# Kernel optimization log

Measured on AMD Instinct MI355X. Metric: run time of the kernel, lower is better.

The kernel has to match this reference:

```python
import jax, jax.numpy as jnp
import numpy as np

DIM_X = 256
DIM_V = 512
DIM_IN = 2
N = 65536
EPS = 0.05          # posdef_tol
CRLB = 0.0          # contraction_rate_lb
STD = 0.5           # weight_init_std


def setup_inputs() -> dict:
    key = jax.random.key(0)
    ks = jax.random.split(key, 8)
    return {
        "t": 0,
        "x": jax.random.normal(ks[0], (N, DIM_X), jnp.float32),
        "Pstar": jax.random.normal(ks[1], (DIM_X, DIM_X), jnp.float32) * STD,
        "Chi": jax.random.normal(ks[2], (DIM_X, DIM_V), jnp.float32) * STD,
        "X": jax.random.normal(ks[3], (DIM_X + DIM_V, DIM_X + DIM_V), jnp.float32) * STD,
        "Y1": jax.random.normal(ks[4], (DIM_X, DIM_X), jnp.float32) * STD,
        "B2": jax.random.normal(ks[5], (DIM_X, DIM_IN), jnp.float32) * STD,
        "D12": jax.random.normal(ks[6], (DIM_V, DIM_IN), jnp.float32) * STD,
        "bv": jnp.zeros((DIM_V,), jnp.float32),
        "bx": jnp.zeros((DIM_X,), jnp.float32),
    }


def _model_matrices(Pstar, Chi, X, Y1):
    """Replicates CREN.update_model_param (F.linear(a,b) == a @ b.T)."""
    dx = Pstar.shape[0]
    P = 0.5 * (Pstar @ Pstar.T) + EPS * jnp.eye(dx, dtype=Pstar.dtype)
    H = X @ X.T + EPS * jnp.eye(X.shape[0], dtype=X.dtype)
    H1 = H[:dx, :dx]
    H2 = H[:dx, dx:]
    H4 = H[dx:, dx:]
    Y = -0.5 * (H1 + CRLB * P + Y1 - Y1.T)
    lam = 0.5 * jnp.diagonal(H4)                 # Lambda is diagonal
    Pinv = jnp.linalg.inv(P)
    A = Pinv @ Y                                  # F.linear(inv(P), Y.T)
    D11 = -jnp.tril(H4, -1) / lam[:, None]        # strictly lower triangular
    C1 = Chi.T / lam[:, None]                     # (dv, dx)
    B1 = Pinv @ (-H2 - Chi)                       # (dx, dv)
    return A, B1, C1, D11


def reference(t, x, Pstar, Chi, X, Y1, B2, D12, bv, bx):
    A, B1, C1, D11 = _model_matrices(Pstar, Chi, X, Y1)
    n = x.shape[0]
    u = jnp.zeros((1, DIM_IN), x.dtype)           # hard-coded zero input in forward
    # precompute the per-step linear terms that do not depend on w:
    # cx[:, i] == F.linear(x, C1[i]) + bv[i] + F.linear(u, D12[i])
    cx = x @ C1.T + bv[None, :] + u @ D12.T       # (n, dv)

    idx = jnp.arange(DIM_V)

    def step(w, xs):
        i, cxi, d_row = xs                        # cxi: (n,), d_row: (dv,)
        v = cxi + w @ d_row                       # forward substitution step
        w = w.at[:, i].set(jnp.tanh(v))
        return w, None

    w0 = jnp.zeros((n, DIM_V), x.dtype)
    w, _ = jax.lax.scan(step, w0, (idx, cx.T, D11))

    x_dot = x @ A.T + w @ B1.T + bx[None, :] + u @ B2.T
    return x_dot


if __name__ == "__main__":
    out = reference(**setup_inputs())
    print(out.shape, out.dtype)
```

## Files before the change

kernel.cpp:

```cpp
#include <hip/hip_runtime.h>
#include <cstdint>
#include <cstddef>

#define DIMX 256
#define DIMV 512
#define DIMH 768
#define EPSV 0.05f

typedef __bf16 bf16x8 __attribute__((ext_vector_type(8)));
typedef unsigned short u16x8 __attribute__((ext_vector_type(8)));
typedef unsigned int u32x4 __attribute__((ext_vector_type(4)));
typedef float f32x4 __attribute__((ext_vector_type(4)));

__device__ __forceinline__ unsigned short f2bf(float f) {
  unsigned int u = __float_as_uint(f);
  u += 0x7fffu + ((u >> 16) & 1u);
  return (unsigned short)(u >> 16);
}
__device__ __forceinline__ float bf2f(unsigned short b) {
  return __uint_as_float(((unsigned int)b) << 16);
}
__device__ __forceinline__ bf16x8 ld8(const unsigned short* p) {
  u16x8 u = *reinterpret_cast<const u16x8*>(p);
  return __builtin_bit_cast(bf16x8, u);
}
__device__ __forceinline__ f32x4 mfma16(bf16x8 a, bf16x8 b, f32x4 c) {
  return __builtin_amdgcn_mfma_f32_16x16x32_bf16(a, b, c, 0, 0, 0);
}
__device__ __forceinline__ float rdlane(float v, int lane) {
  return __uint_as_float(
      (unsigned int)__builtin_amdgcn_readlane((int)__float_as_uint(v), lane));
}

__global__ __launch_bounds__(256) void k_setup1(const float* __restrict__ X,
                                                unsigned short* __restrict__ Xhi,
                                                unsigned short* __restrict__ Xlo,
                                                const float* __restrict__ Pst,
                                                float* __restrict__ P) {
  int blk = blockIdx.x;
  if (blk < 256) {
    int bi = blk >> 4, bj = blk & 15;
    int ty = threadIdx.x >> 4, tx = threadIdx.x & 15;
    int i = bi * 16 + ty, j = bj * 16 + tx;
    const f32x4* ra = reinterpret_cast<const f32x4*>(Pst + (size_t)i * DIMX);
    const f32x4* rb = reinterpret_cast<const f32x4*>(Pst + (size_t)j * DIMX);
    float s = 0.f;
    for (int k = 0; k < 64; ++k) {
      f32x4 a = ra[k], b = rb[k];
      s = fmaf(a[0], b[0], s); s = fmaf(a[1], b[1], s);
      s = fmaf(a[2], b[2], s); s = fmaf(a[3], b[3], s);
    }
    P[(size_t)i * DIMX + j] = 0.5f * s + (i == j ? EPSV : 0.f);
  } else {
    int idx = (blk - 256) * 256 + threadIdx.x;
    if (idx < DIMH * DIMH) {
      float f = X[idx];
      unsigned short h = f2bf(f);
      Xhi[idx] = h;
      Xlo[idx] = f2bf(f - bf2f(h));
    }
  }
}

__global__ __launch_bounds__(256, 1) void k_setup2(float* __restrict__ A,
                                                   float* __restrict__ Wbuf,
                                                   const unsigned short* __restrict__ Xhi,
                                                   const unsigned short* __restrict__ Xlo,
                                                   float* __restrict__ H) {
  __shared__ float Wl[32][33];
  __shared__ float T[32][232];
  if (blockIdx.x == 0) {
    int t = threadIdx.x;
    int wv = t >> 6, l = t & 63;
#pragma unroll 1
    for (int s = 0; s < 8; ++s) {
      int K = 32 * s;
      int R32 = 256 - K - 32;
      if (wv == 0) {
        int li = l & 31;
        float d[32];
#pragma unroll
        for (int j = 0; j < 32; ++j) d[j] = A[(K + j) * 256 + K + li];
#pragma unroll
        for (int k = 0; k < 32; ++k) {
          float dkk = rdlane(d[k], k);
          float ip = rsqrtf(dkk);
          d[k] *= ip;
#pragma unroll
          for (int j = k + 1; j < 32; ++j) {
            float ljk = rdlane(d[k], j);
            d[j] = fmaf(-ljk, d[k], d[j]);
          }
        }
        float wcol[32];
#pragma unroll
        for (int i = 0; i < 32; ++i) {
          float Lii = rdlane(d[i], i);
          float ipi = 1.0f / Lii;
          float acc = (li == i) ? 1.0f : 0.0f;
#pragma unroll
          for (int k = 0; k < i; ++k) {
            float Lik = rdlane(d[k], i);
            acc = fmaf(-Lik, wcol[k], acc);
          }
          wcol[i] = acc * ipi;
        }
        if (l < 32) {
#pragma unroll
          for (int k = 0; k < 32; ++k) {
            Wl[k][l] = wcol[k];
            Wbuf[s * 1024 + k * 32 + l] = wcol[k];
          }
        }
      }
      __syncthreads();
      if (R32 > 0) {
        int nrt = R32 >> 2;
        for (int u = t; u < nrt * 8; u += 256) {
          int rt = u >> 3, jg = u & 7;
          int r = K + 32 + rt * 4;
          int j0 = jg * 4;
          f32x4 z4 = {0.f, 0.f, 0.f, 0.f};
          f32x4 acc[4] = {z4, z4, z4, z4};
#pragma unroll
          for (int k = 0; k < 32; ++k) {
            f32x4 av = *reinterpret_cast<const f32x4*>(&A[(K + k) * 256 + r]);
#pragma unroll
            for (int jj = 0; jj < 4; ++jj) {
              float w = Wl[j0 + jj][k];
              acc[jj][0] = fmaf(av[0], w, acc[jj][0]);
              acc[jj][1] = fmaf(av[1], w, acc[jj][1]);
              acc[jj][2] = fmaf(av[2], w, acc[jj][2]);
              acc[jj][3] = fmaf(av[3], w, acc[jj][3]);
            }
          }
#pragma unroll
          for (int jj = 0; jj < 4; ++jj)
            *reinterpret_cast<f32x4*>(&T[j0 + jj][rt * 4]) = acc[jj];
        }
        __syncthreads();
#pragma unroll 1
        for (int j = 0; j < 32; ++j) {
          int rl = t << 2;
          if (rl < R32)
            *reinterpret_cast<f32x4*>(&A[(K + j) * 256 + K + 32 + rl]) =
                *reinterpret_cast<const f32x4*>(&T[j][rl]);
        }
        int T4 = R32 >> 2;
        int ntile = T4 * (T4 + 1) / 2;
        for (int idx = t; idx < ntile; idx += 256) {
          int ti = (int)((sqrtf(8.0f * (float)idx + 1.0f) - 1.0f) * 0.5f);
          while ((ti + 1) * (ti + 2) / 2 <= idx) ++ti;
          while (ti * (ti + 1) / 2 > idx) --ti;
          int tj = idx - ti * (ti + 1) / 2;
          int gi = K + 32 + 4 * ti, gj = K + 32 + 4 * tj;
          f32x4 acc[4];
#pragma unroll
          for (int jj = 0; jj < 4; ++jj)
            acc[jj] = *reinterpret_cast<const f32x4*>(&A[(gj + jj) * 256 + gi]);
#pragma unroll
          for (int k = 0; k < 32; ++k) {
            f32x4 av = *reinterpret_cast<const f32x4*>(&T[k][4 * ti]);
            f32x4 bv = *reinterpret_cast<const f32x4*>(&T[k][4 * tj]);
#pragma unroll
            for (int jj = 0; jj < 4; ++jj) {
              acc[jj][0] = fmaf(-av[0], bv[jj], acc[jj][0]);
              acc[jj][1] = fmaf(-av[1], bv[jj], acc[jj][1]);
              acc[jj][2] = fmaf(-av[2], bv[jj], acc[jj][2]);
              acc[jj][3] = fmaf(-av[3], bv[jj], acc[jj][3]);
            }
          }
#pragma unroll
          for (int jj = 0; jj < 4; ++jj)
            *reinterpret_cast<f32x4*>(&A[(gj + jj) * 256 + gi]) = acc[jj];
        }
      }
      __syncthreads();
    }
  } else {
    int b2 = blockIdx.x - 1;
    int bx = b2 % 12, by = b2 / 12;
    int i0 = by * 64, j0 = bx * 64;
    int l = threadIdx.x & 63, wv = threadIdx.x >> 6;
    int lr = l & 15, lq = l >> 4;
    int koff = lq * 8;
    int arow = i0 + wv * 16 + lr;
    f32x4 z = {0.f, 0.f, 0.f, 0.f};
    f32x4 acc[4] = {z, z, z, z};
    for (int pass = 0; pass < 3; ++pass) {
      const unsigned short* Xa = (pass == 2) ? Xlo : Xhi;
      const unsigned short* Xb = (pass == 1) ? Xlo : Xhi;
      for (int kc = 0; kc < 24; ++kc) {
        bf16x8 a = ld8(&Xa[(size_t)arow * DIMH + kc * 32 + koff]);
#pragma unroll
        for (int ct = 0; ct < 4; ++ct) {
          bf16x8 b = ld8(&Xb[(size_t)(j0 + ct * 16 + lr) * DIMH + kc * 32 + koff]);
          acc[ct] = mfma16(a, b, acc[ct]);
        }
      }
    }
#pragma unroll
    for (int ct = 0; ct < 4; ++ct)
#pragma unroll
      for (int r = 0; r < 4; ++r) {
        int i = i0 + wv * 16 + lq * 4 + r;
        int j = j0 + ct * 16 + lr;
        H[(size_t)i * DIMH + j] = acc[ct][r] + (i == j ? EPSV : 0.f);
      }
  }
}

__global__ __launch_bounds__(256, 2) void k_setup3(const float* __restrict__ H,
                                                   const float* __restrict__ Chi,
                                                   unsigned short* __restrict__ Gin,
                                                   const float* __restrict__ Lg,
                                                   const float* __restrict__ Wbuf,
                                                   const float* __restrict__ Y1,
                                                   unsigned short* __restrict__ Gout) {
  __shared__ float Bs[256][33];
  __shared__ float Wl[32][33];
  int blk = blockIdx.x;
  if (blk < 1536) {
    int xb = blk % 3, c = blk / 3;
    int q = xb * 256 + threadIdx.x;
    float rlam = 2.f / H[(size_t)(256 + c) * DIMH + 256 + c];
    float v;
    if (q < 256) {
      v = Chi[(size_t)q * DIMV + c] * rlam;
    } else {
      int j = q - 256;
      v = (j < c) ? -H[(size_t)(256 + c) * DIMH + 256 + j] * rlam : 0.f;
    }
    Gin[(size_t)c * DIMH + q] = f2bf(v);
    return;
  }
  int bq = blk - 1536;
  int t = threadIdx.x, tc = t & 31, rg = t >> 5;
  int q = bq * 32 + tc;
#pragma unroll 1
  for (int rr = 0; rr < 32; ++rr) {
    int r = rg * 32 + rr;
    float v;
    if (q < 256) {
      v = -0.5f * (H[(size_t)r * DIMH + q] + Y1[r * 256 + q] - Y1[q * 256 + r]);
    } else {
      int c = q - 256;
      v = -(H[(size_t)r * DIMH + 256 + c] + Chi[r * 512 + c]);
    }
    Bs[r][tc] = v;
  }
  __syncthreads();
#pragma unroll 1
  for (int s = 0; s < 8; ++s) {
    for (int idx = t; idx < 1024; idx += 256) Wl[idx >> 5][idx & 31] = Wbuf[s * 1024 + idx];
    __syncthreads();
    float ua[4] = {0.f, 0.f, 0.f, 0.f};
#pragma unroll
    for (int k = 0; k < 32; ++k) {
      float b = Bs[32 * s + k][tc];
#pragma unroll
      for (int rr = 0; rr < 4; ++rr) ua[rr] = fmaf(Wl[rg * 4 + rr][k], b, ua[rr]);
    }
    __syncthreads();
#pragma unroll
    for (int rr = 0; rr < 4; ++rr) Bs[32 * s + rg * 4 + rr][tc] = ua[rr];
    __syncthreads();
#pragma unroll 1
    for (int rb = 32 * (s + 1) + rg * 4; rb < 256; rb += 32) {
      f32x4 acc = {Bs[rb][tc], Bs[rb + 1][tc], Bs[rb + 2][tc], Bs[rb + 3][tc]};
#pragma unroll
      for (int k = 0; k < 32; ++k) {
        float u = Bs[32 * s + k][tc];
        f32x4 lv = *reinterpret_cast<const f32x4*>(&Lg[(32 * s + k) * 256 + rb]);
        acc[0] = fmaf(-lv[0], u, acc[0]);
        acc[1] = fmaf(-lv[1], u, acc[1]);
        acc[2] = fmaf(-lv[2], u, acc[2]);
        acc[3] = fmaf(-lv[3], u, acc[3]);
      }
      Bs[rb][tc] = acc[0]; Bs[rb + 1][tc] = acc[1];
      Bs[rb + 2][tc] = acc[2]; Bs[rb + 3][tc] = acc[3];
    }
    __syncthreads();
  }
#pragma unroll 1
  for (int s = 7; s >= 0; --s) {
    for (int idx = t; idx < 1024; idx += 256) Wl[idx >> 5][idx & 31] = Wbuf[s * 1024 + idx];
    __syncthreads();
    float ga[4] = {0.f, 0.f, 0.f, 0.f};
#pragma unroll
    for (int k = 0; k < 32; ++k) {
      float b = Bs[32 * s + k][tc];
#pragma unroll
      for (int rr = 0; rr < 4; ++rr) ga[rr] = fmaf(Wl[k][rg * 4 + rr], b, ga[rr]);
    }
    __syncthreads();
#pragma unroll
    for (int rr = 0; rr < 4; ++rr) Bs[32 * s + rg * 4 + rr][tc] = ga[rr];
    __syncthreads();
    if (s > 0) {
#pragma unroll 1
      for (int rb = rg * 4; rb < 32 * s; rb += 32) {
        f32x4 acc = {Bs[rb][tc], Bs[rb + 1][tc], Bs[rb + 2][tc], Bs[rb + 3][tc]};
#pragma unroll
        for (int kq = 0; kq < 8; ++kq) {
          f32x4 l0 = *reinterpret_cast<const f32x4*>(&Lg[(rb + 0) * 256 + 32 * s + 4 * kq]);
          f32x4 l1 = *reinterpret_cast<const f32x4*>(&Lg[(rb + 1) * 256 + 32 * s + 4 * kq]);
          f32x4 l2 = *reinterpret_cast<const f32x4*>(&Lg[(rb + 2) * 256 + 32 * s + 4 * kq]);
          f32x4 l3 = *reinterpret_cast<const f32x4*>(&Lg[(rb + 3) * 256 + 32 * s + 4 * kq]);
#pragma unroll
          for (int e = 0; e < 4; ++e) {
            float g = Bs[32 * s + 4 * kq + e][tc];
            acc[0] = fmaf(-l0[e], g, acc[0]);
            acc[1] = fmaf(-l1[e], g, acc[1]);
            acc[2] = fmaf(-l2[e], g, acc[2]);
            acc[3] = fmaf(-l3[e], g, acc[3]);
          }
        }
        Bs[rb][tc] = acc[0]; Bs[rb + 1][tc] = acc[1];
        Bs[rb + 2][tc] = acc[2]; Bs[rb + 3][tc] = acc[3];
      }
    }
    __syncthreads();
  }
#pragma unroll 1
  for (int rr = 0; rr < 32; ++rr) {
    int r = rg * 32 + rr;
    Gout[(size_t)r * DIMH + q] = f2bf(Bs[r][tc]);
  }
}

#define ACCSTR 33
#define ACC_W 4224
#define DD_W 2048
#define WT_W 2560
#define SMEM_MAIN (4 * (ACC_W + DD_W + WT_W))

__global__ __launch_bounds__(256, 2) void k_main(const float* __restrict__ x,
                                                 const unsigned short* __restrict__ Gin,
                                                 const unsigned short* __restrict__ Gout,
                                                 const float* __restrict__ bv,
                                                 const float* __restrict__ bx,
                                                 float* __restrict__ out) {
  extern __shared__ char smem[];
  int tid = threadIdx.x;
  int wv = tid >> 6, l = tid & 63;
  int lr = l & 15, lq = l >> 4, koff = lq * 8;
  float* accb = (float*)(smem + wv * ACC_W);
  char* ddiag = smem + 4 * ACC_W + wv * DD_W;
  char* wtmp = smem + 4 * ACC_W + 4 * DD_W + wv * WT_W;

  int rowbase = blockIdx.x * 128 + wv * 32;

  bf16x8 frag0[24], frag1[24];
  {
    u16x8 zz = {0, 0, 0, 0, 0, 0, 0, 0};
#pragma unroll
    for (int c = 8; c < 24; ++c) {
      frag0[c] = __builtin_bit_cast(bf16x8, zz);
      frag1[c] = __builtin_bit_cast(bf16x8, zz);
    }
  }
#pragma unroll
  for (int kc = 0; kc < 8; ++kc) {
    const float* xr0 = x + (size_t)(rowbase + lr) * 256 + koff + kc * 32;
    const float* xr1 = x + (size_t)(rowbase + 16 + lr) * 256 + koff + kc * 32;
    f32x4 a0 = *reinterpret_cast<const f32x4*>(xr0);
    f32x4 a1 = *reinterpret_cast<const f32x4*>(xr0 + 4);
    f32x4 b0 = *reinterpret_cast<const f32x4*>(xr1);
    f32x4 b1 = *reinterpret_cast<const f32x4*>(xr1 + 4);
    u16x8 u0, u1;
#pragma unroll
    for (int e = 0; e < 4; ++e) {
      u0[e] = f2bf(a0[e]); u0[4 + e] = f2bf(a1[e]);
      u1[e] = f2bf(b0[e]); u1[4 + e] = f2bf(b1[e]);
    }
    frag0[kc] = __builtin_bit_cast(bf16x8, u0);
    frag1[kc] = __builtin_bit_cast(bf16x8, u1);
  }

  f32x4 z = {0.f, 0.f, 0.f, 0.f};

#pragma unroll 1
  for (int b = 0; b < 16; ++b) {
#pragma unroll
    for (int t = 0; t < 2; ++t) {
      int row = t * 16 + (l >> 2);
      const unsigned short* src =
          Gin + (size_t)(32 * b + row) * DIMH + 256 + 32 * b + (l & 3) * 8;
      u16x8 v = *reinterpret_cast<const u16x8*>(src);
      *reinterpret_cast<u16x8*>(ddiag + t * 1024 + l * 16) = v;
    }

    f32x4 a00 = z, a01 = z, a10 = z, a11 = z;
    const unsigned short* gb0 = Gin + (size_t)(32 * b + lr) * DIMH + koff;
    const unsigned short* gb1 = gb0 + 16 * DIMH;
#pragma unroll
    for (int g = 0; g < 6; ++g) {
      if (g * 4 < 8 + b) {
#pragma unroll
        for (int cc = 0; cc < 4; ++cc) {
          int c = g * 4 + cc;
          bf16x8 bb0 = ld8(gb0 + c * 32);
          bf16x8 bb1 = ld8(gb1 + c * 32);
          a00 = mfma16(frag0[c], bb0, a00);
          a01 = mfma16(frag0[c], bb1, a01);
          a10 = mfma16(frag1[c], bb0, a10);
          a11 = mfma16(frag1[c], bb1, a11);
        }
      }
    }

    float bv0 = bv[32 * b + lr], bv1 = bv[32 * b + 16 + lr];
#pragma unroll
    for (int r = 0; r < 4; ++r) {
      accb[(lq * 4 + r) * ACCSTR + lr] = a00[r] + bv0;
      accb[(lq * 4 + r) * ACCSTR + 16 + lr] = a01[r] + bv1;
      accb[(16 + lq * 4 + r) * ACCSTR + lr] = a10[r] + bv0;
      accb[(16 + lq * 4 + r) * ACCSTR + 16 + lr] = a11[r] + bv1;
    }

    if (l < 32) {
      const unsigned int* dd = (const unsigned int*)ddiag;
      unsigned int* wrow = (unsigned int*)(wtmp + l * 80);
      float wf[32];
      unsigned int cur = 0;
#pragma unroll
      for (int i = 0; i < 32; ++i) {
        float p0 = 0.f, p1 = 0.f;
        const unsigned int* ddr = dd + i * 16;
#pragma unroll
        for (int j = 0; j < i; ++j) {
          unsigned int pw = ddr[j >> 1];
          float dj = __uint_as_float((j & 1) ? (pw & 0xffff0000u) : (pw << 16));
          if (j & 1) p1 = fmaf(dj, wf[j], p1);
          else       p0 = fmaf(dj, wf[j], p0);
        }
        float s = accb[l * ACCSTR + i] + p0 + p1;
        float e = __builtin_amdgcn_exp2f(s * 2.885390082f);
        float w = fmaf(-2.f, __builtin_amdgcn_rcpf(e + 1.f), 1.f);
        wf[i] = w;
        unsigned int hb = (unsigned int)f2bf(w);
        if (i & 1) { cur |= hb << 16; wrow[i >> 1] = cur; }
        else       cur = hb;
      }
    }

    bf16x8 nw0 = ld8((const unsigned short*)(wtmp + lr * 80 + lq * 16));
    bf16x8 nw1 = ld8((const unsigned short*)(wtmp + (16 + lr) * 80 + lq * 16));
#pragma unroll
    for (int j = 0; j < 16; ++j) {
      if (b == j) { frag0[8 + j] = nw0; frag1[8 + j] = nw1; }
    }
  }

#pragma unroll 1
  for (int ct = 0; ct < 16; ++ct) {
    f32x4 o0 = z, o1 = z;
    const unsigned short* gg = Gout + (size_t)(ct * 16 + lr) * DIMH + koff;
#pragma unroll
    for (int c = 0; c < 24; ++c) {
      bf16x8 bb = ld8(gg + c * 32);
      o0 = mfma16(frag0[c], bb, o0);
      o1 = mfma16(frag1[c], bb, o1);
    }
    float bxv = bx[ct * 16 + lr];
#pragma unroll
    for (int r = 0; r < 4; ++r) {
      out[(size_t)(rowbase + lq * 4 + r) * 256 + ct * 16 + lr] = o0[r] + bxv;
      out[(size_t)(rowbase + 16 + lq * 4 + r) * 256 + ct * 16 + lr] = o1[r] + bxv;
    }
  }
}

extern "C" void kernel_launch(void* const* d_in, const int* in_sizes, int n_in,
                              void* d_out, int out_size, void* d_ws, size_t ws_size,
                              hipStream_t stream) {
  const float* x   = (const float*)d_in[1];
  const float* Pst = (const float*)d_in[2];
  const float* Chi = (const float*)d_in[3];
  const float* X   = (const float*)d_in[4];
  const float* Y1  = (const float*)d_in[5];
  const float* bv  = (const float*)d_in[8];
  const float* bx  = (const float*)d_in[9];
  float* out = (float*)d_out;

  char* ws = (char*)d_ws;
  const size_t OFF_H    = 0;
  const size_t OFF_P    = 2359296;
  const size_t OFF_WB   = 2621440;
  const size_t OFF_XHI  = 2883584;
  const size_t OFF_XLO  = 4063232;
  const size_t OFF_GIN  = 5242880;
  const size_t OFF_GOUT = 6029312;
  if (ws_size < 6422528) return;

  float* H    = (float*)(ws + OFF_H);
  float* P    = (float*)(ws + OFF_P);
  float* Wbuf = (float*)(ws + OFF_WB);
  unsigned short* Xhi  = (unsigned short*)(ws + OFF_XHI);
  unsigned short* Xlo  = (unsigned short*)(ws + OFF_XLO);
  unsigned short* Gin  = (unsigned short*)(ws + OFF_GIN);
  unsigned short* Gout = (unsigned short*)(ws + OFF_GOUT);

  k_setup1<<<2560, 256, 0, stream>>>(X, Xhi, Xlo, Pst, P);
  k_setup2<<<145, 256, 0, stream>>>(P, Wbuf, Xhi, Xlo, H);
  k_setup3<<<1560, 256, 0, stream>>>(H, Chi, Gin, P, Wbuf, Y1, Gout);
  k_main<<<512, 256, SMEM_MAIN, stream>>>(x, Gin, Gout, bv, bx, out);
}
```

Baseline: 716.1 us.

## Replace per-column triangular solves with explicit Cholesky inverse and parallel GEMM

```diff
diff --git a/kernel.cpp b/kernel.cpp
--- a/kernel.cpp
+++ b/kernel.cpp
@@ -63,12 +63,13 @@
 }
 
 __global__ __launch_bounds__(256, 1) void k_setup2(float* __restrict__ A,
-                                                   float* __restrict__ Wbuf,
+                                                   float* __restrict__ Li,
                                                    const unsigned short* __restrict__ Xhi,
                                                    const unsigned short* __restrict__ Xlo,
                                                    float* __restrict__ H) {
   __shared__ float Wl[32][33];
   __shared__ float T[32][232];
+  __shared__ float Lp2[224][33];
   if (blockIdx.x == 0) {
     int t = threadIdx.x;
     int wv = t >> 6, l = t & 63;
@@ -109,7 +110,7 @@
 #pragma unroll
           for (int k = 0; k < 32; ++k) {
             Wl[k][l] = wcol[k];
-            Wbuf[s * 1024 + k * 32 + l] = wcol[k];
+            Li[(32 * s + k) * 256 + 32 * s + l] = wcol[k];
           }
         }
       }
@@ -174,6 +175,69 @@
           for (int jj = 0; jj < 4; ++jj)
             *reinterpret_cast<f32x4*>(&A[(gj + jj) * 256 + gi]) = acc[jj];
         }
+      }
+      __syncthreads();
+    }
+
+    float* Tb = &T[0][0];
+#pragma unroll 1
+    for (int i = 1; i < 8; ++i) {
+      for (int idx = t; idx < 32 * 32 * i; idx += 256) {
+        int r = idx & 31, cc = idx >> 5;
+        Lp2[cc][r] = A[cc * 256 + 32 * i + r];
+      }
+      for (int idx = t; idx < 1024; idx += 256) {
+        int r = idx >> 5, kk = idx & 31;
+        Wl[r][kk] = Li[(32 * i + r) * 256 + 32 * i + kk];
+      }
+      __syncthreads();
+      int nt1 = i * 64;
+      for (int u = t; u < nt1; u += 256) {
+        int j = u >> 6, v = u & 63;
+        int r0 = (v >> 3) * 4, c0 = (v & 7) * 4;
+        f32x4 z4 = {0.f, 0.f, 0.f, 0.f};
+        f32x4 acc[4] = {z4, z4, z4, z4};
+        for (int k = j; k < i; ++k) {
+#pragma unroll
+          for (int kk = 0; kk < 32; ++kk) {
+            f32x4 lv = *reinterpret_cast<const f32x4*>(
+                &Li[(32 * k + kk) * 256 + 32 * j + c0]);
+#pragma unroll
+            for (int e = 0; e < 4; ++e) {
+              float lpe = Lp2[32 * k + kk][r0 + e];
+              acc[e][0] = fmaf(lpe, lv[0], acc[e][0]);
+              acc[e][1] = fmaf(lpe, lv[1], acc[e][1]);
+              acc[e][2] = fmaf(lpe, lv[2], acc[e][2]);
+              acc[e][3] = fmaf(lpe, lv[3], acc[e][3]);
+            }
+          }
+        }
+#pragma unroll
+        for (int e = 0; e < 4; ++e)
+          *reinterpret_cast<f32x4*>(&Tb[j * 1024 + (r0 + e) * 32 + c0]) = acc[e];
+      }
+      __syncthreads();
+      for (int u = t; u < nt1; u += 256) {
+        int j = u >> 6, v = u & 63;
+        int r0 = (v >> 3) * 4, c0 = (v & 7) * 4;
+        f32x4 z4 = {0.f, 0.f, 0.f, 0.f};
+        f32x4 acc[4] = {z4, z4, z4, z4};
+#pragma unroll
+        for (int kk = 0; kk < 32; ++kk) {
+          f32x4 tv = *reinterpret_cast<const f32x4*>(&Tb[j * 1024 + kk * 32 + c0]);
+#pragma unroll
+          for (int e = 0; e < 4; ++e) {
+            float w = Wl[r0 + e][kk];
+            acc[e][0] = fmaf(-w, tv[0], acc[e][0]);
+            acc[e][1] = fmaf(-w, tv[1], acc[e][1]);
+            acc[e][2] = fmaf(-w, tv[2], acc[e][2]);
+            acc[e][3] = fmaf(-w, tv[3], acc[e][3]);
+          }
+        }
+#pragma unroll
+        for (int e = 0; e < 4; ++e)
+          *reinterpret_cast<f32x4*>(&Li[(32 * i + r0 + e) * 256 + 32 * j + c0]) =
+              acc[e];
       }
       __syncthreads();
     }
@@ -213,120 +277,92 @@
 __global__ __launch_bounds__(256, 2) void k_setup3(const float* __restrict__ H,
                                                    const float* __restrict__ Chi,
                                                    unsigned short* __restrict__ Gin,
-                                                   const float* __restrict__ Lg,
-                                                   const float* __restrict__ Wbuf,
-                                                   const float* __restrict__ Y1,
-                                                   unsigned short* __restrict__ Gout) {
-  __shared__ float Bs[256][33];
-  __shared__ float Wl[32][33];
+                                                   const float* __restrict__ Li,
+                                                   float* __restrict__ Pinv) {
   int blk = blockIdx.x;
-  if (blk < 1536) {
-    int xb = blk % 3, c = blk / 3;
-    int q = xb * 256 + threadIdx.x;
-    float rlam = 2.f / H[(size_t)(256 + c) * DIMH + 256 + c];
-    float v;
-    if (q < 256) {
-      v = Chi[(size_t)q * DIMV + c] * rlam;
-    } else {
-      int j = q - 256;
-      v = (j < c) ? -H[(size_t)(256 + c) * DIMH + 256 + j] * rlam : 0.f;
-    }
-    Gin[(size_t)c * DIMH + q] = f2bf(v);
+  int t = threadIdx.x;
+  if (blk < 36) {
+    int bi = (int)((sqrtf(8.0f * (float)blk + 1.0f) - 1.0f) * 0.5f);
+    while ((bi + 1) * (bi + 2) / 2 <= blk) ++bi;
+    while (bi * (bi + 1) / 2 > blk) --bi;
+    int bj = blk - bi * (bi + 1) / 2;
+    int r = t >> 3, c0 = (t & 7) * 4;
+    f32x4 acc = {0.f, 0.f, 0.f, 0.f};
+    for (int kb = bi; kb < 8; ++kb) {
+#pragma unroll
+      for (int kk = 0; kk < 32; ++kk) {
+        float a = Li[(32 * kb + kk) * 256 + 32 * bi + r];
+        f32x4 b = *reinterpret_cast<const f32x4*>(
+            &Li[(32 * kb + kk) * 256 + 32 * bj + c0]);
+        acc[0] = fmaf(a, b[0], acc[0]);
+        acc[1] = fmaf(a, b[1], acc[1]);
+        acc[2] = fmaf(a, b[2], acc[2]);
+        acc[3] = fmaf(a, b[3], acc[3]);
+      }
+    }
+    *reinterpret_cast<f32x4*>(&Pinv[(32 * bi + r) * 256 + 32 * bj + c0]) = acc;
+    if (bi != bj) {
+#pragma unroll
+      for (int e = 0; e < 4; ++e)
+        Pinv[(32 * bj + c0 + e) * 256 + 32 * bi + r] = acc[e];
+    }
     return;
   }
-  int bq = blk - 1536;
-  int t = threadIdx.x, tc = t & 31, rg = t >> 5;
-  int q = bq * 32 + tc;
-#pragma unroll 1
-  for (int rr = 0; rr < 32; ++rr) {
-    int r = rg * 32 + rr;
-    float v;
-    if (q < 256) {
-      v = -0.5f * (H[(size_t)r * DIMH + q] + Y1[r * 256 + q] - Y1[q * 256 + r]);
-    } else {
-      int c = q - 256;
-      v = -(H[(size_t)r * DIMH + 256 + c] + Chi[r * 512 + c]);
-    }
-    Bs[r][tc] = v;
-  }
-  __syncthreads();
-#pragma unroll 1
-  for (int s = 0; s < 8; ++s) {
-    for (int idx = t; idx < 1024; idx += 256) Wl[idx >> 5][idx & 31] = Wbuf[s * 1024 + idx];
+  int b2 = blk - 36;
+  int xb = b2 % 3, c = b2 / 3;
+  int q = xb * 256 + t;
+  float rlam = 2.f / H[(size_t)(256 + c) * DIMH + 256 + c];
+  float v;
+  if (q < 256) {
+    v = Chi[(size_t)q * DIMV + c] * rlam;
+  } else {
+    int j = q - 256;
+    v = (j < c) ? -H[(size_t)(256 + c) * DIMH + 256 + j] * rlam : 0.f;
+  }
+  Gin[(size_t)c * DIMH + q] = f2bf(v);
+}
+
+__global__ __launch_bounds__(256) void k_gout(const float* __restrict__ Pinv,
+                                              const float* __restrict__ H,
+                                              const float* __restrict__ Y1,
+                                              const float* __restrict__ Chi,
+                                              unsigned short* __restrict__ Gout) {
+  __shared__ float Ps[32][33], Bs[32][33];
+  int q0 = blockIdx.x * 32, i0 = blockIdx.y * 32;
+  int t = threadIdx.x;
+  int tx = t & 31, ty = t >> 5;
+  int lrr = t >> 3, lc4 = (t & 7) * 4;
+  float acc[4] = {0.f, 0.f, 0.f, 0.f};
+  for (int kc = 0; kc < 8; ++kc) {
+    int k0 = kc * 32;
+    f32x4 pv = *reinterpret_cast<const f32x4*>(&Pinv[(size_t)(i0 + lrr) * 256 + k0 + lc4]);
+    Ps[lrr][lc4 + 0] = pv[0]; Ps[lrr][lc4 + 1] = pv[1];
+    Ps[lrr][lc4 + 2] = pv[2]; Ps[lrr][lc4 + 3] = pv[3];
+    int k = k0 + lrr;
+#pragma unroll
+    for (int e = 0; e < 4; ++e) {
+      int q = q0 + lc4 + e;
+      float v;
+      if (q < 256) {
+        v = -0.5f * (H[(size_t)k * DIMH + q] + Y1[(size_t)k * 256 + q] - Y1[(size_t)q * 256 + k]);
+      } else {
+        int c = q - 256;
+        v = -(H[(size_t)k * DIMH + 256 + c] + Chi[(size_t)k * DIMV + c]);
+      }
+      Bs[lrr][lc4 + e] = v;
+    }
     __syncthreads();
-    float ua[4] = {0.f, 0.f, 0.f, 0.f};
-#pragma unroll
-    for (int k = 0; k < 32; ++k) {
-      float b = Bs[32 * s + k][tc];
-#pragma unroll
-      for (int rr = 0; rr < 4; ++rr) ua[rr] = fmaf(Wl[rg * 4 + rr][k], b, ua[rr]);
+#pragma unroll
+    for (int kk = 0; kk < 32; ++kk) {
+      float bb = Bs[kk][tx];
+#pragma unroll
+      for (int rr = 0; rr < 4; ++rr) acc[rr] = fmaf(Ps[4 * ty + rr][kk], bb, acc[rr]);
     }
     __syncthreads();
-#pragma unroll
-    for (int rr = 0; rr < 4; ++rr) Bs[32 * s + rg * 4 + rr][tc] = ua[rr];
-    __syncthreads();
-#pragma unroll 1
-    for (int rb = 32 * (s + 1) + rg * 4; rb < 256; rb += 32) {
-      f32x4 acc = {Bs[rb][tc], Bs[rb + 1][tc], Bs[rb + 2][tc], Bs[rb + 3][tc]};
-#pragma unroll
-      for (int k = 0; k < 32; ++k) {
-        float u = Bs[32 * s + k][tc];
-        f32x4 lv = *reinterpret_cast<const f32x4*>(&Lg[(32 * s + k) * 256 + rb]);
-        acc[0] = fmaf(-lv[0], u, acc[0]);
-        acc[1] = fmaf(-lv[1], u, acc[1]);
-        acc[2] = fmaf(-lv[2], u, acc[2]);
-        acc[3] = fmaf(-lv[3], u, acc[3]);
-      }
-      Bs[rb][tc] = acc[0]; Bs[rb + 1][tc] = acc[1];
-      Bs[rb + 2][tc] = acc[2]; Bs[rb + 3][tc] = acc[3];
-    }
-    __syncthreads();
-  }
-#pragma unroll 1
-  for (int s = 7; s >= 0; --s) {
-    for (int idx = t; idx < 1024; idx += 256) Wl[idx >> 5][idx & 31] = Wbuf[s * 1024 + idx];
-    __syncthreads();
-    float ga[4] = {0.f, 0.f, 0.f, 0.f};
-#pragma unroll
-    for (int k = 0; k < 32; ++k) {
-      float b = Bs[32 * s + k][tc];
-#pragma unroll
-      for (int rr = 0; rr < 4; ++rr) ga[rr] = fmaf(Wl[k][rg * 4 + rr], b, ga[rr]);
-    }
-    __syncthreads();
-#pragma unroll
-    for (int rr = 0; rr < 4; ++rr) Bs[32 * s + rg * 4 + rr][tc] = ga[rr];
-    __syncthreads();
-    if (s > 0) {
-#pragma unroll 1
-      for (int rb = rg * 4; rb < 32 * s; rb += 32) {
-        f32x4 acc = {Bs[rb][tc], Bs[rb + 1][tc], Bs[rb + 2][tc], Bs[rb + 3][tc]};
-#pragma unroll
-        for (int kq = 0; kq < 8; ++kq) {
-          f32x4 l0 = *reinterpret_cast<const f32x4*>(&Lg[(rb + 0) * 256 + 32 * s + 4 * kq]);
-          f32x4 l1 = *reinterpret_cast<const f32x4*>(&Lg[(rb + 1) * 256 + 32 * s + 4 * kq]);
-          f32x4 l2 = *reinterpret_cast<const f32x4*>(&Lg[(rb + 2) * 256 + 32 * s + 4 * kq]);
-          f32x4 l3 = *reinterpret_cast<const f32x4*>(&Lg[(rb + 3) * 256 + 32 * s + 4 * kq]);
-#pragma unroll
-          for (int e = 0; e < 4; ++e) {
-            float g = Bs[32 * s + 4 * kq + e][tc];
-            acc[0] = fmaf(-l0[e], g, acc[0]);
-            acc[1] = fmaf(-l1[e], g, acc[1]);
-            acc[2] = fmaf(-l2[e], g, acc[2]);
-            acc[3] = fmaf(-l3[e], g, acc[3]);
-          }
-        }
-        Bs[rb][tc] = acc[0]; Bs[rb + 1][tc] = acc[1];
-        Bs[rb + 2][tc] = acc[2]; Bs[rb + 3][tc] = acc[3];
-      }
-    }
-    __syncthreads();
-  }
-#pragma unroll 1
-  for (int rr = 0; rr < 32; ++rr) {
-    int r = rg * 32 + rr;
-    Gout[(size_t)r * DIMH + q] = f2bf(Bs[r][tc]);
-  }
+  }
+#pragma unroll
+  for (int rr = 0; rr < 4; ++rr)
+    Gout[(size_t)(i0 + 4 * ty + rr) * DIMH + q0 + tx] = f2bf(acc[rr]);
 }
 
 #define ACCSTR 33
@@ -487,7 +523,6 @@
   char* ws = (char*)d_ws;
   const size_t OFF_H    = 0;
   const size_t OFF_P    = 2359296;
-  const size_t OFF_WB   = 2621440;
   const size_t OFF_XHI  = 2883584;
   const size_t OFF_XLO  = 4063232;
   const size_t OFF_GIN  = 5242880;
@@ -496,14 +531,16 @@
 
   float* H    = (float*)(ws + OFF_H);
   float* P    = (float*)(ws + OFF_P);
-  float* Wbuf = (float*)(ws + OFF_WB);
+  float* Li   = (float*)(ws + OFF_GOUT);
   unsigned short* Xhi  = (unsigned short*)(ws + OFF_XHI);
   unsigned short* Xlo  = (unsigned short*)(ws + OFF_XLO);
   unsigned short* Gin  = (unsigned short*)(ws + OFF_GIN);
   unsigned short* Gout = (unsigned short*)(ws + OFF_GOUT);
 
   k_setup1<<<2560, 256, 0, stream>>>(X, Xhi, Xlo, Pst, P);
-  k_setup2<<<145, 256, 0, stream>>>(P, Wbuf, Xhi, Xlo, H);
-  k_setup3<<<1560, 256, 0, stream>>>(H, Chi, Gin, P, Wbuf, Y1, Gout);
+  k_setup2<<<145, 256, 0, stream>>>(P, Li, Xhi, Xlo, H);
+  k_setup3<<<1572, 256, 0, stream>>>(H, Chi, Gin, Li, P);
+  dim3 go(24, 8);
+  k_gout<<<go, 256, 0, stream>>>(P, H, Y1, Chi, Gout);
   k_main<<<512, 256, SMEM_MAIN, stream>>>(x, Gin, Gout, bv, bx, out);
 }
```

Result: faster. 606.3 us (median of 2 runs) (-15.3%).
